# Kernel tuning notes

Measured on AMD Instinct MI355X. Metric: run time of the kernel, lower is better.

## Reference

```python
import jax, jax.numpy as jnp
import numpy as np

K = 8          # number of TR cores / modes
D = 1024       # categories per mode
R = 64         # TR rank
NDRAWS = 2048
EPS = 1e-30


def setup_inputs() -> dict:
    key = jax.random.key(0)
    ks = jax.random.split(key, K)
    inp = {f"log_core{i}": jax.random.normal(ks[i], (D, R, R), dtype=jnp.float32)
           for i in range(K)}
    inp["n_draws"] = NDRAWS
    return inp


def _sample(cores, n_draws, seed=1):
    """Batched version of trip_index_sample: all draws sampled in parallel."""
    k = len(cores)
    # heads[j] = S_0 @ ... @ S_{j-1} with S_i = core_i.sum(0); heads[0] = None
    heads = [None]
    acc = cores[0].sum(axis=0)
    for c in cores[1:]:
        heads.append(acc)
        acc = acc @ c.sum(axis=0)
    norm = acc  # S_0 ... S_{K-1}

    keys = jax.random.split(jax.random.key(seed), k)
    tail = None          # [B, r_{j+1}, r_K] running suffix product per draw
    idxs = []
    for step, j in enumerate(range(k - 1, -1, -1)):
        core, head = cores[j], heads[j]
        if tail is None:
            # first step (j = K-1): marginal weights shared by all draws
            if head is None:  # degenerate K == 1 case
                w = jnp.trace(core, axis1=1, axis2=2)
            else:
                w = jnp.einsum('ab,nba->n', head, core)
            ix = jax.random.categorical(keys[step], jnp.log(jnp.clip(w, EPS)),
                                        shape=(n_draws,))
            tail = core[ix]  # [B, r_j, r_K]
        else:
            # M = tail @ head : [B, r_{j+1}, r_j] (head is None only at j == 0,
            # where r_0 == r_K so tail already has the right shape)
            M = tail if head is None else tail @ head
            w = jnp.einsum('nab,Bba->Bn', core, M)  # [B, d_j]
            ix = jax.random.categorical(keys[step], jnp.log(jnp.clip(w, EPS)),
                                        axis=-1)
            tail = jnp.einsum('Bab,Bbc->Bac', core[ix], tail)
        idxs.append(ix)
    sample = jnp.stack(idxs[::-1], axis=1)  # [B, K], mode order 0..K-1
    log_p = jnp.log(jnp.clip(jnp.trace(tail, axis1=1, axis2=2), EPS)) \
            - jnp.log(jnp.trace(norm))
    return sample, log_p


def reference(log_core0, log_core1, log_core2, log_core3,
              log_core4, log_core5, log_core6, log_core7, n_draws):
    log_cores = [log_core0, log_core1, log_core2, log_core3,
                 log_core4, log_core5, log_core6, log_core7]
    cores = [jax.nn.softplus(c) for c in log_cores]
    sample, log_p = _sample(cores, n_draws)
    return sample, log_p
```

## Files before the change

### kernel.cpp

```cpp
#include <hip/hip_runtime.h>
#include <stdint.h>
#include <math.h>

#define D_CAT  1024
#define R_TR   64
#define RR     4096
#define NDRAWS 2048
#define KMODES 8

struct CorePtrs { const float* p[KMODES]; };

typedef __attribute__((ext_vector_type(8))) __bf16 bf16x8;
typedef __attribute__((ext_vector_type(4))) float  f32x4;
typedef unsigned int u32;

union BF8 { ushort u[8]; bf16x8 v; };

static __device__ inline void async_cp16(const void* g, void* l) {
  __builtin_amdgcn_global_load_lds(
      (const __attribute__((address_space(1))) u32*)g,
      (__attribute__((address_space(3))) u32*)l, 16, 0, 0);
}

static __host__ __device__ inline uint32_t rotl32(uint32_t x, int r) {
  return (x << r) | (x >> (32 - r));
}
static __host__ __device__ inline void tf2x32(uint32_t k1, uint32_t k2,
                                              uint32_t x0, uint32_t x1,
                                              uint32_t& o0, uint32_t& o1) {
  uint32_t ks0 = k1, ks1 = k2, ks2 = k1 ^ k2 ^ 0x1BD11BDAu;
  x0 += ks0; x1 += ks1;
  x0 += x1; x1 = rotl32(x1, 13); x1 ^= x0;
  x0 += x1; x1 = rotl32(x1, 15); x1 ^= x0;
  x0 += x1; x1 = rotl32(x1, 26); x1 ^= x0;
  x0 += x1; x1 = rotl32(x1, 6);  x1 ^= x0;
  x0 += ks1; x1 += ks2 + 1u;
  x0 += x1; x1 = rotl32(x1, 17); x1 ^= x0;
  x0 += x1; x1 = rotl32(x1, 29); x1 ^= x0;
  x0 += x1; x1 = rotl32(x1, 16); x1 ^= x0;
  x0 += x1; x1 = rotl32(x1, 24); x1 ^= x0;
  x0 += ks2; x1 += ks0 + 2u;
  x0 += x1; x1 = rotl32(x1, 13); x1 ^= x0;
  x0 += x1; x1 = rotl32(x1, 15); x1 ^= x0;
  x0 += x1; x1 = rotl32(x1, 26); x1 ^= x0;
  x0 += x1; x1 = rotl32(x1, 6);  x1 ^= x0;
  x0 += ks0; x1 += ks1 + 3u;
  x0 += x1; x1 = rotl32(x1, 17); x1 ^= x0;
  x0 += x1; x1 = rotl32(x1, 29); x1 ^= x0;
  x0 += x1; x1 = rotl32(x1, 16); x1 ^= x0;
  x0 += x1; x1 = rotl32(x1, 24); x1 ^= x0;
  x0 += ks1; x1 += ks2 + 4u;
  x0 += x1; x1 = rotl32(x1, 13); x1 ^= x0;
  x0 += x1; x1 = rotl32(x1, 15); x1 ^= x0;
  x0 += x1; x1 = rotl32(x1, 26); x1 ^= x0;
  x0 += x1; x1 = rotl32(x1, 6);  x1 ^= x0;
  x0 += ks2; x1 += ks0 + 5u;
  o0 = x0; o1 = x1;
}

static __device__ inline float softplus_fast(float x) {
  float e = __expf(-fabsf(x));
  return fmaxf(x, 0.0f) + __logf(1.0f + e);
}

static __device__ inline unsigned short f32_bf16(float f) {
  uint32_t u = __float_as_uint(f);
  u += 0x7fffu + ((u >> 16) & 1u);
  return (unsigned short)(u >> 16);
}

static __device__ inline float gumbel_at(uint32_t k1, uint32_t k2, uint32_t e) {
  uint32_t o0, o1;
  tf2x32(k1, k2, 0u, e, o0, o1);
  uint32_t bits = o0 ^ o1;
  float f = __uint_as_float((bits >> 9) | 0x3F800000u) - 1.0f;
  float u = (f > 0.0f) ? f : 1.17549435e-38f;
  return -logf(-logf(u));
}


__global__ void k_sentinel(float* out, int n) {
  int i = blockIdx.x * 256 + threadIdx.x;
  if (i < n) out[i] = -12288.0f;
}

__global__ __launch_bounds__(256) void k_spart(CorePtrs cp, float* __restrict__ Spart) {
  const int bid = blockIdx.x, tid = threadIdx.x;
  const int i = bid >> 8, c = bid & 255;
  const float* src = cp.p[i] + (size_t)c * 4 * RR;
  float acc[16];
#pragma unroll
  for (int k = 0; k < 16; ++k) acc[k] = 0.0f;
#pragma unroll
  for (int d = 0; d < 4; ++d) {
    const float* row = src + (size_t)d * RR;
#pragma unroll
    for (int k = 0; k < 16; ++k)
      acc[k] += softplus_fast(row[tid + k * 256]);
  }
  float* dst = Spart + (size_t)bid * RR;
#pragma unroll
  for (int k = 0; k < 16; ++k) dst[tid + k * 256] = acc[k];
}

__global__ __launch_bounds__(256) void k_sreduce(const float* __restrict__ Spart,
                                                 double* __restrict__ S) {
  const int idx = blockIdx.x * 256 + threadIdx.x;
  const int i = idx >> 12, rr = idx & 4095;
  const float* p = Spart + ((size_t)i << 20) + rr;
  double a0 = 0.0, a1 = 0.0, a2 = 0.0, a3 = 0.0;
  for (int c = 0; c < 256; c += 4) {
    a0 += (double)p[(size_t)(c + 0) * RR];
    a1 += (double)p[(size_t)(c + 1) * RR];
    a2 += (double)p[(size_t)(c + 2) * RR];
    a3 += (double)p[(size_t)(c + 3) * RR];
  }
  S[idx] = (a0 + a1) + (a2 + a3);
}

__global__ __launch_bounds__(256) void k_heads(const double* __restrict__ S,
                                               double* __restrict__ heads,
                                               double* __restrict__ misc) {
  __shared__ double cur[RR];
  __shared__ double Sm[RR];
  __shared__ double tbuf[64];
  const int tid = threadIdx.x;
  const int bcol = tid & 63;
  const int a0 = tid >> 6;
#pragma unroll
  for (int k = 0; k < 16; ++k) {
    int p = tid + k * 256;
    double v = S[p];
    cur[p] = v;
    heads[p] = v;
  }
  __syncthreads();
  for (int m = 1; m <= 6; ++m) {
#pragma unroll
    for (int k = 0; k < 16; ++k) {
      int p = tid + k * 256;
      Sm[p] = S[(size_t)m * RR + p];
    }
    __syncthreads();
    double acc[16];
#pragma unroll
    for (int k = 0; k < 16; ++k) acc[k] = 0.0;
    for (int c = 0; c < 64; ++c) {
      double s = Sm[c * 64 + bcol];
#pragma unroll
      for (int k = 0; k < 16; ++k)
        acc[k] = fma(cur[(a0 + 4 * k) * 64 + c], s, acc[k]);
    }
    __syncthreads();
#pragma unroll
    for (int k = 0; k < 16; ++k) {
      int p = tid + k * 256;
      cur[p] = acc[k];
      heads[(size_t)m * RR + p] = acc[k];
    }
    __syncthreads();
  }
#pragma unroll
  for (int k = 0; k < 16; ++k) {
    int p = tid + k * 256;
    Sm[p] = S[(size_t)7 * RR + p];
  }
  __syncthreads();
  if (tid < 64) {
    double acc = 0.0;
    for (int c = 0; c < 64; ++c)
      acc = fma(cur[tid * 64 + c], Sm[c * 64 + tid], acc);
    tbuf[tid] = acc;
  }
  __syncthreads();
  if (tid == 0) {
    double tr = 0.0;
    for (int a = 0; a < 64; ++a) tr += tbuf[a];
    misc[0] = log(tr);
  }
}

__global__ __launch_bounds__(256) void k_w0(const float* __restrict__ raw,
                                            const double* __restrict__ head7,
                                            float* __restrict__ W) {
  const int tid = threadIdx.x;
  const int lane = tid & 63;
  const int n = blockIdx.x * 4 + (tid >> 6);
  const float* crow = raw + (size_t)n * RR;
  double acc = 0.0;
  for (int q = lane; q < RR; q += 64)
    acc = fma((double)softplus_fast(crow[q]), head7[(q & 63) * 64 + (q >> 6)], acc);
  for (int m = 32; m; m >>= 1) acc += __shfl_xor(acc, m);
  if (lane == 0) W[n] = (float)acc;
}

__global__ __launch_bounds__(256) void k_spmt(const float* __restrict__ src,
                                              ushort* __restrict__ Bh,
                                              ushort* __restrict__ Bl,
                                              const float* __restrict__ tail,
                                              const double* __restrict__ head, int useHead,
                                              ushort* __restrict__ Ah,
                                              ushort* __restrict__ Al) {
  __shared__ alignas(16) float smem[4176];
  const int bid = blockIdx.x, tid = threadIdx.x;
  if (bid < 4096) {
    const size_t i4 = ((size_t)bid * 256 + tid) * 4;
    float4 v = *(const float4*)(src + i4);
    const float ov[4] = {softplus_fast(v.x), softplus_fast(v.y),
                         softplus_fast(v.z), softplus_fast(v.w)};
    ushort h4[4], l4[4];
#pragma unroll
    for (int q = 0; q < 4; ++q) {
      ushort h = f32_bf16(ov[q]);
      float hf = __uint_as_float((uint32_t)h << 16);
      h4[q] = h;
      l4[q] = f32_bf16(ov[q] - hf);
    }
    *(ushort4*)(Bh + i4) = make_ushort4(h4[0], h4[1], h4[2], h4[3]);
    *(ushort4*)(Bl + i4) = make_ushort4(l4[0], l4[1], l4[2], l4[3]);
    return;
  }
  const int blk = bid - 4096;
  if (useHead) {
    ushort (*hT)[4096] = (ushort(*)[4096])smem;
#pragma unroll
    for (int rep = 0; rep < 16; ++rep) {
      int i = tid + rep * 256;
      float v = (float)head[(i & 63) * 64 + (i >> 6)];
      ushort h = f32_bf16(v);
      float hf = __uint_as_float((uint32_t)h << 16);
      int dst = (i & 0xFC0) | (((((i >> 3) & 7) ^ ((i >> 6) & 7)) << 3)) | (i & 7);
      hT[0][dst] = h;
      hT[1][dst] = f32_bf16(v - hf);
    }
    __syncthreads();
    const int w = tid >> 6, l = tid & 63;
    const int B = blk * 4 + w;
    const float* tb = tail + (size_t)B * RR;
    const int lrow = l & 15, kg = l >> 4;
    ushort* ah_out = Ah + (size_t)B * RR;
    ushort* al_out = Al + (size_t)B * RR;
    for (int it = 0; it < 4; ++it) {
      BF8 afh[2], afl[2];
#pragma unroll
      for (int kt = 0; kt < 2; ++kt) {
        const float* s2 = tb + (it * 16 + lrow) * 64 + kt * 32 + kg * 8;
        float4 v0 = *(const float4*)s2;
        float4 v1 = *(const float4*)(s2 + 4);
        float vv[8] = {v0.x, v0.y, v0.z, v0.w, v1.x, v1.y, v1.z, v1.w};
#pragma unroll
        for (int q = 0; q < 8; ++q) {
          ushort h = f32_bf16(vv[q]);
          float hf = __uint_as_float((uint32_t)h << 16);
          afh[kt].u[q] = h;
          afl[kt].u[q] = f32_bf16(vv[q] - hf);
        }
      }
#pragma unroll
      for (int kt2 = 0; kt2 < 4; ++kt2) {
        f32x4 hh = (f32x4)0.0f, sm = (f32x4)0.0f;
#pragma unroll
        for (int kt = 0; kt < 2; ++kt) {
          int rowB = kt2 * 16 + lrow;
          int kcA  = kt * 4 + kg;
          int off  = rowB * 64 + ((kcA ^ (rowB & 7)) << 3);
          bf16x8 bh = *(const bf16x8*)&hT[0][off];
          bf16x8 bl = *(const bf16x8*)&hT[1][off];
          hh = __builtin_amdgcn_mfma_f32_16x16x32_bf16(afh[kt].v, bh, hh, 0, 0, 0);
          sm = __builtin_amdgcn_mfma_f32_16x16x32_bf16(afh[kt].v, bl, sm, 0, 0, 0);
          sm = __builtin_amdgcn_mfma_f32_16x16x32_bf16(afl[kt].v, bh, sm, 0, 0, 0);
        }
        ushort h4[4], l4[4];
#pragma unroll
        for (int q = 0; q < 4; ++q) {
          float v = hh[q] + sm[q];
          ushort h = f32_bf16(v);
          float hf = __uint_as_float((uint32_t)h << 16);
          h4[q] = h;
          l4[q] = f32_bf16(v - hf);
        }
        int o = (kt2 * 16 + lrow) * 64 + it * 16 + kg * 4;
        *(ushort4*)(ah_out + o) = make_ushort4(h4[0], h4[1], h4[2], h4[3]);
        *(ushort4*)(al_out + o) = make_ushort4(l4[0], l4[1], l4[2], l4[3]);
      }
    }
  } else {
    float* tl = smem;
    for (int d = 0; d < 4; ++d) {
      const int B = blk * 4 + d;
      const float* tb = tail + (size_t)B * RR;
      ushort* ah_out = Ah + (size_t)B * RR;
      ushort* al_out = Al + (size_t)B * RR;
      __syncthreads();
#pragma unroll
      for (int r = 0; r < 4; ++r) {
        int p = tid * 4 + r * 1024;
        int i = p >> 6, k = p & 63;
        float4 v = *(const float4*)(tb + p);
        tl[i * 65 + k + 0] = v.x; tl[i * 65 + k + 1] = v.y;
        tl[i * 65 + k + 2] = v.z; tl[i * 65 + k + 3] = v.w;
      }
      __syncthreads();
#pragma unroll
      for (int r = 0; r < 4; ++r) {
        int p = tid * 4 + r * 1024;
        int k = p >> 6, i0 = p & 63;
        ushort h4[4], l4[4];
#pragma unroll
        for (int q = 0; q < 4; ++q) {
          float m = tl[(i0 + q) * 65 + k];
          ushort h = f32_bf16(m);
          float hf = __uint_as_float((uint32_t)h << 16);
          h4[q] = h;
          l4[q] = f32_bf16(m - hf);
        }
        *(ushort4*)(ah_out + p) = make_ushort4(h4[0], h4[1], h4[2], h4[3]);
        *(ushort4*)(al_out + p) = make_ushort4(l4[0], l4[1], l4[2], l4[3]);
      }
    }
  }
}

__global__ __launch_bounds__(256) void k_wgemm(const ushort* __restrict__ Ah,
                                               const ushort* __restrict__ Al,
                                               const ushort* __restrict__ Bh,
                                               const ushort* __restrict__ Bl,
                                               float* __restrict__ W) {
  __shared__ ushort lds[2][4 * 4096];
  const int tid = threadIdx.x;
  const int L = blockIdx.x;
  const int x = L & 7, j = L >> 3;
  const int bn = (x & 1) * 8 + (j & 7);
  const int bb = (x >> 1) * 8 + (j >> 3);
  const int w = tid >> 6, l = tid & 63;

  const int srow = l >> 3;
  const int skc  = l & 7;
  const ushort* gbase;
  {
    const ushort* bases[4] = {Ah + (size_t)bb * 64 * RR, Al + (size_t)bb * 64 * RR,
                              Bh + (size_t)bn * 64 * RR, Bl + (size_t)bn * 64 * RR};
    gbase = bases[w] + (size_t)srow * RR + (size_t)((skc ^ srow) * 8);
  }

  const int wm = (w >> 1) * 32, wn = (w & 1) * 32;
  const int lrow = l & 15;
  const int kg   = l >> 4;

  f32x4 acc_hh[2][2], acc_sm[2][2], hht[2][2];
#pragma unroll
  for (int mt = 0; mt < 2; ++mt)
#pragma unroll
    for (int nt = 0; nt < 2; ++nt) {
      acc_hh[mt][nt] = (f32x4)0.0f;
      acc_sm[mt][nt] = (f32x4)0.0f;
      hht[mt][nt]    = (f32x4)0.0f;
    }

  int roffA[2][2], roffB[2][2];
#pragma unroll
  for (int mt = 0; mt < 2; ++mt)
#pragma unroll
    for (int kt = 0; kt < 2; ++kt) {
      int rowA = wm + mt * 16 + lrow;
      int kcA  = kt * 4 + kg;
      roffA[mt][kt] = rowA * 64 + ((kcA ^ (rowA & 7)) << 3);
      int rowB = wn + mt * 16 + lrow;
      roffB[mt][kt] = rowB * 64 + ((kcA ^ (rowB & 7)) << 3);
    }

#pragma unroll
  for (int q = 0; q < 8; ++q)
    async_cp16(gbase + (size_t)q * 8 * RR, &lds[0][w * 4096 + q * 512]);

  for (int t = 0; t < 64; ++t) {
    const int bf = t & 1;
    __syncthreads();
    if (t < 63) {
      const int koff = (t + 1) * 64;
#pragma unroll
      for (int q = 0; q < 8; ++q)
        async_cp16(gbase + (size_t)q * 8 * RR + koff,
                   &lds[bf ^ 1][w * 4096 + q * 512]);
    }
    const ushort* L2 = lds[bf];
#pragma unroll
    for (int kt = 0; kt < 2; ++kt) {
      bf16x8 ah[2], al[2], bh[2], bl[2];
#pragma unroll
      for (int mt = 0; mt < 2; ++mt) {
        ah[mt] = *(const bf16x8*)&L2[0 * 4096 + roffA[mt][kt]];
        al[mt] = *(const bf16x8*)&L2[1 * 4096 + roffA[mt][kt]];
      }
#pragma unroll
      for (int nt = 0; nt < 2; ++nt) {
        bh[nt] = *(const bf16x8*)&L2[2 * 4096 + roffB[nt][kt]];
        bl[nt] = *(const bf16x8*)&L2[3 * 4096 + roffB[nt][kt]];
      }
#pragma unroll
      for (int mt = 0; mt < 2; ++mt)
#pragma unroll
        for (int nt = 0; nt < 2; ++nt) {
          acc_hh[mt][nt] = __builtin_amdgcn_mfma_f32_16x16x32_bf16(ah[mt], bh[nt], acc_hh[mt][nt], 0, 0, 0);
          acc_sm[mt][nt] = __builtin_amdgcn_mfma_f32_16x16x32_bf16(ah[mt], bl[nt], acc_sm[mt][nt], 0, 0, 0);
          acc_sm[mt][nt] = __builtin_amdgcn_mfma_f32_16x16x32_bf16(al[mt], bh[nt], acc_sm[mt][nt], 0, 0, 0);
        }
    }
    if ((t & 15) == 15) {
#pragma unroll
      for (int mt = 0; mt < 2; ++mt)
#pragma unroll
        for (int nt = 0; nt < 2; ++nt) {
          hht[mt][nt] += acc_hh[mt][nt];
          acc_hh[mt][nt] = (f32x4)0.0f;
        }
    }
  }

#pragma unroll
  for (int mt = 0; mt < 2; ++mt)
#pragma unroll
    for (int nt = 0; nt < 2; ++nt)
#pragma unroll
      for (int q = 0; q < 4; ++q) {
        int gr = bb * 64 + wm + mt * 16 + kg * 4 + q;
        int gc = bn * 64 + wn + nt * 16 + lrow;
        W[(size_t)gr * D_CAT + gc] = hht[mt][nt][q] + acc_sm[mt][nt][q];
      }
}

__global__ __launch_bounds__(256) void k_samptail(const float* __restrict__ W, int shared_row,
                                                  uint32_t key1, uint32_t key2,
                                                  float* __restrict__ out, int mode_j,
                                                  const float* __restrict__ raw,
                                                  const ushort* __restrict__ Bh,
                                                  const ushort* __restrict__ Bl,
                                                  float* __restrict__ tail, int first) {
  __shared__ float sv[4];
  __shared__ int   si[4];
  __shared__ int   s_m;
  __shared__ alignas(16) ushort Th[4096];
  __shared__ alignas(16) ushort Tl[4096];
  const int b = blockIdx.x, tid = threadIdx.x;

  {
    const float* wrow = W + (shared_row ? 0 : (size_t)b * D_CAT);
    float best = -3.4e38f; int bidx = 0x7fffffff;
    for (int k = 0; k < 4; ++k) {
      int n = tid + k * 256;
      float lg = logf(fmaxf(wrow[n], 1e-30f));
      float v = gumbel_at(key1, key2, (uint32_t)(b * D_CAT + n)) + lg;
      if (v > best || (v == best && n < bidx)) { best = v; bidx = n; }
    }
    for (int m = 32; m; m >>= 1) {
      float ov = __shfl_xor(best, m);
      int   oi = __shfl_xor(bidx, m);
      if (ov > best || (ov == best && oi < bidx)) { best = ov; bidx = oi; }
    }
    if ((tid & 63) == 0) { sv[tid >> 6] = best; si[tid >> 6] = bidx; }
    __syncthreads();
    if (tid == 0) {
      for (int t = 1; t < 4; ++t)
        if (sv[t] > best || (sv[t] == best && si[t] < bidx)) { best = sv[t]; bidx = si[t]; }
      s_m = bidx;
      out[b * KMODES + mode_j] = (float)bidx;
    }
    __syncthreads();
  }
  const int m = s_m;
  float* trow = tail + (size_t)b * RR;

  if (first) {
    const float* crow = raw + (size_t)m * RR;
#pragma unroll
    for (int r = 0; r < 4; ++r) {
      float4 v = *(const float4*)(crow + tid * 4 + r * 1024);
      float4 o;
      o.x = softplus_fast(v.x); o.y = softplus_fast(v.y);
      o.z = softplus_fast(v.z); o.w = softplus_fast(v.w);
      *(float4*)(trow + tid * 4 + r * 1024) = o;
    }
    return;
  }
  const ushort* ch = Bh + (size_t)m * RR;
  const ushort* cl = Bl + (size_t)m * RR;

#pragma unroll
  for (int r = 0; r < 4; ++r) {
    int p = tid * 4 + r * 1024;
    int i = p >> 6, k = p & 63;
    float4 v = *(const float4*)(trow + p);
    float vv[4] = {v.x, v.y, v.z, v.w};
#pragma unroll
    for (int q = 0; q < 4; ++q) {
      int row = k + q;
      int dst = row * 64 + ((((i >> 3) ^ (row & 7)) << 3)) + (i & 7);
      ushort h = f32_bf16(vv[q]);
      float hf = __uint_as_float((uint32_t)h << 16);
      Th[dst] = h;
      Tl[dst] = f32_bf16(vv[q] - hf);
    }
  }
  __syncthreads();

  const int w = tid >> 6, l = tid & 63;
  const int lrow = l & 15, kg = l >> 4;
  bf16x8 ah[2], al[2];
#pragma unroll
  for (int kt = 0; kt < 2; ++kt) {
    int off = (w * 16 + lrow) * 64 + kt * 32 + kg * 8;
    ah[kt] = *(const bf16x8*)(ch + off);
    al[kt] = *(const bf16x8*)(cl + off);
  }
#pragma unroll
  for (int jt = 0; jt < 4; ++jt) {
    f32x4 hh = (f32x4)0.0f, sm = (f32x4)0.0f;
#pragma unroll
    for (int kt = 0; kt < 2; ++kt) {
      int rowB = jt * 16 + lrow;
      int kcA  = kt * 4 + kg;
      int off  = rowB * 64 + ((kcA ^ (rowB & 7)) << 3);
      bf16x8 bh = *(const bf16x8*)&Th[off];
      bf16x8 bl = *(const bf16x8*)&Tl[off];
      hh = __builtin_amdgcn_mfma_f32_16x16x32_bf16(ah[kt], bh, hh, 0, 0, 0);
      sm = __builtin_amdgcn_mfma_f32_16x16x32_bf16(ah[kt], bl, sm, 0, 0, 0);
      sm = __builtin_amdgcn_mfma_f32_16x16x32_bf16(al[kt], bh, sm, 0, 0, 0);
      sm = __builtin_amdgcn_mfma_f32_16x16x32_bf16(al[kt], bl, sm, 0, 0, 0);
    }
#pragma unroll
    for (int q = 0; q < 4; ++q)
      trow[(w * 16 + kg * 4 + q) * 64 + jt * 16 + lrow] = hh[q] + sm[q];
  }
}

__global__ __launch_bounds__(256) void k_logp(const float* __restrict__ tail,
                                              const double* __restrict__ misc,
                                              float* __restrict__ out) {
  const int b = blockIdx.x * 256 + threadIdx.x;
  double tr = 0.0;
  for (int a = 0; a < 64; ++a) tr += (double)tail[(size_t)b * RR + a * 65];
  double lp = log(fmax(tr, 1e-30)) - misc[0];
  out[NDRAWS * KMODES + b] = (float)lp;
}

extern "C" void kernel_launch(void* const* d_in, const int* in_sizes, int n_in,
                              void* d_out, int out_size, void* d_ws, size_t ws_size,
                              hipStream_t stream) {
  (void)in_sizes; (void)n_in;
  CorePtrs cp;
  for (int i = 0; i < KMODES; ++i) cp.p[i] = (const float*)d_in[i];
  float* outf = (float*)d_out;

  char* base = (char*)d_ws;
  const size_t o_w     = 0;
  const size_t o_tail  = o_w + (size_t)NDRAWS * D_CAT * 4;
  const size_t o_ahl   = o_tail + (size_t)NDRAWS * RR * 4;
  const size_t o_spart = o_ahl;
  const size_t o_S     = o_ahl + (size_t)NDRAWS * RR * 4;
  const size_t o_heads = o_S + (size_t)KMODES * RR * 8;
  const size_t o_misc  = o_heads + (size_t)7 * RR * 8;
  const size_t o_bh    = o_misc + 256;
  const size_t o_bl    = o_bh + (size_t)D_CAT * RR * 2;
  const size_t NEED    = o_bl + (size_t)D_CAT * RR * 2;
  if (ws_size < NEED) {
    k_sentinel<<<(out_size + 255) / 256, 256, 0, stream>>>(outf, out_size);
    return;
  }

  float*  W     = (float*)(base + o_w);
  float*  tail  = (float*)(base + o_tail);
  ushort* Ah    = (ushort*)(base + o_ahl);
  ushort* Al    = Ah + (size_t)NDRAWS * RR;
  float*  Spart = (float*)(base + o_spart);
  double* S     = (double*)(base + o_S);
  double* heads = (double*)(base + o_heads);
  double* misc  = (double*)(base + o_misc);
  ushort* Bh    = (ushort*)(base + o_bh);
  ushort* Bl    = (ushort*)(base + o_bl);

  uint32_t kk1[KMODES], kk2[KMODES];
  for (uint32_t s = 0; s < KMODES; ++s) tf2x32(0u, 1u, 0u, s, kk1[s], kk2[s]);

  k_spart  <<<2048, 256, 0, stream>>>(cp, Spart);
  k_sreduce<<<128,  256, 0, stream>>>(Spart, S);
  k_heads  <<<1,    256, 0, stream>>>(S, heads, misc);

  for (int s = 0; s < KMODES; ++s) {
    const int j = 7 - s;
    if (s == 0) {
      k_w0<<<256, 256, 0, stream>>>(cp.p[7], heads + (size_t)6 * RR, W);
    } else {
      k_spmt<<<4608, 256, 0, stream>>>(cp.p[j], Bh, Bl, tail,
                                       j > 0 ? heads + (size_t)(j - 1) * RR : heads,
                                       j > 0 ? 1 : 0, Ah, Al);
      k_wgemm<<<512, 256, 0, stream>>>(Ah, Al, Bh, Bl, W);
    }
    k_samptail<<<NDRAWS, 256, 0, stream>>>(W, s == 0 ? 1 : 0, kk1[s], kk2[s],
                                           outf, j, cp.p[j], Bh, Bl, tail,
                                           s == 0 ? 1 : 0);
  }
  k_logp<<<KMODES, 256, 0, stream>>>(tail, misc, outf);
}
```

Before: 866.8 us.

## Split wgemm K-dimension across two block halves and drop LDS double buffering

The W GEMM grid doubles to 1024 blocks. Each half handles half of the 4096-long reduction dimension and writes a separate partial W buffer, and the sampling kernel adds the two partials before taking the log. The LDS double buffer is replaced by a single buffer with synchronous load-then-compute, which halves shared memory to allow more resident blocks and improve occupancy on the 256-CU device. The costs are lost load/compute overlap within a block, an extra 8 MB partial buffer written and read each step, and a slightly different summation order for the hh accumulation.

```diff
diff --git a/kernel.cpp b/kernel.cpp
--- a/kernel.cpp
+++ b/kernel.cpp
@@ -326,10 +326,12 @@
                                                const ushort* __restrict__ Bh,
                                                const ushort* __restrict__ Bl,
                                                float* __restrict__ W) {
-  __shared__ ushort lds[2][4 * 4096];
+  __shared__ ushort lds[4 * 4096];
   const int tid = threadIdx.x;
   const int L = blockIdx.x;
-  const int x = L & 7, j = L >> 3;
+  const int half = L >> 9;
+  const int r = L & 511;
+  const int x = r & 7, j = r >> 3;
   const int bn = (x & 1) * 8 + (j & 7);
   const int bb = (x >> 1) * 8 + (j >> 3);
   const int w = tid >> 6, l = tid & 63;
@@ -340,7 +342,8 @@
   {
     const ushort* bases[4] = {Ah + (size_t)bb * 64 * RR, Al + (size_t)bb * 64 * RR,
                               Bh + (size_t)bn * 64 * RR, Bl + (size_t)bn * 64 * RR};
-    gbase = bases[w] + (size_t)srow * RR + (size_t)((skc ^ srow) * 8);
+    gbase = bases[w] + (size_t)srow * RR + (size_t)((skc ^ srow) * 8)
+          + (size_t)half * 2048;
   }
 
   const int wm = (w >> 1) * 32, wn = (w & 1) * 32;
@@ -369,33 +372,24 @@
       roffB[mt][kt] = rowB * 64 + ((kcA ^ (rowB & 7)) << 3);
     }
 
-#pragma unroll
-  for (int q = 0; q < 8; ++q)
-    async_cp16(gbase + (size_t)q * 8 * RR, &lds[0][w * 4096 + q * 512]);
-
-  for (int t = 0; t < 64; ++t) {
-    const int bf = t & 1;
-    __syncthreads();
-    if (t < 63) {
-      const int koff = (t + 1) * 64;
-#pragma unroll
-      for (int q = 0; q < 8; ++q)
-        async_cp16(gbase + (size_t)q * 8 * RR + koff,
-                   &lds[bf ^ 1][w * 4096 + q * 512]);
-    }
-    const ushort* L2 = lds[bf];
+  for (int t = 0; t < 32; ++t) {
+    __syncthreads();
+#pragma unroll
+    for (int q = 0; q < 8; ++q)
+      async_cp16(gbase + (size_t)q * 8 * RR + t * 64, &lds[w * 4096 + q * 512]);
+    __syncthreads();
 #pragma unroll
     for (int kt = 0; kt < 2; ++kt) {
       bf16x8 ah[2], al[2], bh[2], bl[2];
 #pragma unroll
       for (int mt = 0; mt < 2; ++mt) {
-        ah[mt] = *(const bf16x8*)&L2[0 * 4096 + roffA[mt][kt]];
-        al[mt] = *(const bf16x8*)&L2[1 * 4096 + roffA[mt][kt]];
+        ah[mt] = *(const bf16x8*)&lds[0 * 4096 + roffA[mt][kt]];
+        al[mt] = *(const bf16x8*)&lds[1 * 4096 + roffA[mt][kt]];
       }
 #pragma unroll
       for (int nt = 0; nt < 2; ++nt) {
-        bh[nt] = *(const bf16x8*)&L2[2 * 4096 + roffB[nt][kt]];
-        bl[nt] = *(const bf16x8*)&L2[3 * 4096 + roffB[nt][kt]];
+        bh[nt] = *(const bf16x8*)&lds[2 * 4096 + roffB[nt][kt]];
+        bl[nt] = *(const bf16x8*)&lds[3 * 4096 + roffB[nt][kt]];
       }
 #pragma unroll
       for (int mt = 0; mt < 2; ++mt)
@@ -417,6 +411,7 @@
     }
   }
 
+  float* Wout = W + (size_t)half * NDRAWS * D_CAT;
 #pragma unroll
   for (int mt = 0; mt < 2; ++mt)
 #pragma unroll
@@ -425,7 +420,7 @@
       for (int q = 0; q < 4; ++q) {
         int gr = bb * 64 + wm + mt * 16 + kg * 4 + q;
         int gc = bn * 64 + wn + nt * 16 + lrow;
-        W[(size_t)gr * D_CAT + gc] = hht[mt][nt][q] + acc_sm[mt][nt][q];
+        Wout[(size_t)gr * D_CAT + gc] = hht[mt][nt][q] + acc_sm[mt][nt][q];
       }
 }
 
@@ -444,11 +439,13 @@
   const int b = blockIdx.x, tid = threadIdx.x;
 
   {
-    const float* wrow = W + (shared_row ? 0 : (size_t)b * D_CAT);
+    const float* w0row = W + (shared_row ? 0 : (size_t)b * D_CAT);
+    const float* w1row = W + (size_t)NDRAWS * D_CAT + (size_t)b * D_CAT;
     float best = -3.4e38f; int bidx = 0x7fffffff;
     for (int k = 0; k < 4; ++k) {
       int n = tid + k * 256;
-      float lg = logf(fmaxf(wrow[n], 1e-30f));
+      float wv = shared_row ? w0row[n] : (w0row[n] + w1row[n]);
+      float lg = logf(fmaxf(wv, 1e-30f));
       float v = gumbel_at(key1, key2, (uint32_t)(b * D_CAT + n)) + lg;
       if (v > best || (v == best && n < bidx)) { best = v; bidx = n; }
     }
@@ -553,7 +550,7 @@
 
   char* base = (char*)d_ws;
   const size_t o_w     = 0;
-  const size_t o_tail  = o_w + (size_t)NDRAWS * D_CAT * 4;
+  const size_t o_tail  = o_w + (size_t)2 * NDRAWS * D_CAT * 4;
   const size_t o_ahl   = o_tail + (size_t)NDRAWS * RR * 4;
   const size_t o_spart = o_ahl;
   const size_t o_S     = o_ahl + (size_t)NDRAWS * RR * 4;
@@ -593,7 +590,7 @@
       k_spmt<<<4608, 256, 0, stream>>>(cp.p[j], Bh, Bl, tail,
                                        j > 0 ? heads + (size_t)(j - 1) * RR : heads,
                                        j > 0 ? 1 : 0, Ah, Al);
-      k_wgemm<<<512, 256, 0, stream>>>(Ah, Al, Bh, Bl, W);
+      k_wgemm<<<1024, 256, 0, stream>>>(Ah, Al, Bh, Bl, W);
     }
     k_samptail<<<NDRAWS, 256, 0, stream>>>(W, s == 0 ? 1 : 0, kk1[s], kk2[s],
                                            outf, j, cp.p[j], Bh, Bl, tail,
```

After: 880.0 us. No clear change (+1.5%).
